# Kernel optimization log

Hardware: AMD Instinct MI355X
Metric: run time of the kernel (lower is better)

Reference implementation:

```python
import jax, jax.numpy as jnp
import numpy as np

B, S, D, H, F = 2, 2048, 1024, 16, 4096
DH = D // H
EPS = 1e-6


def layer_norm(x, g, b):
    mu = jnp.mean(x, axis=-1, keepdims=True)
    var = jnp.mean(jnp.square(x - mu), axis=-1, keepdims=True)
    return (x - mu) * jax.lax.rsqrt(var + EPS) * g + b


def setup_inputs() -> dict:
    key = jax.random.key(0)
    ks = jax.random.split(key, 12)
    s_in = 1.0 / np.sqrt(D)
    s_ff = 1.0 / np.sqrt(F)
    return {
        "x_enc": jax.random.normal(ks[0], (B, S, D), jnp.float32),
        "x_pos": jax.random.normal(ks[1], (B, S, D), jnp.float32),
        "wq": jax.random.normal(ks[2], (D, D), jnp.float32) * s_in,
        "bq": jnp.zeros((D,), jnp.float32),
        "wk": jax.random.normal(ks[3], (D, D), jnp.float32) * s_in,
        "bk": jnp.zeros((D,), jnp.float32),
        "wv": jax.random.normal(ks[4], (D, D), jnp.float32) * s_in,
        "bv": jnp.zeros((D,), jnp.float32),
        "wc": jax.random.normal(ks[5], (D, D), jnp.float32) * s_in,
        "bc": jnp.zeros((D,), jnp.float32),
        "w1": jax.random.normal(ks[6], (D, F), jnp.float32) * s_in,
        "b1": jnp.zeros((F,), jnp.float32),
        "w2": jax.random.normal(ks[7], (F, D), jnp.float32) * s_ff,
        "b2": jnp.zeros((D,), jnp.float32),
        "g1": jnp.ones((D,), jnp.float32),
        "be1": jnp.zeros((D,), jnp.float32),
        "g2": jnp.ones((D,), jnp.float32),
        "be2": jnp.zeros((D,), jnp.float32),
    }


def reference(x_enc, x_pos, wq, bq, wk, bk, wv, bv, wc, bc, w1, b1, w2, b2, g1, be1, g2, be2):
    x = x_enc + x_pos  # [B,S,D]

    def split_heads(t):  # [B,S,D] -> [B,H,S,DH]
        return t.reshape(B, S, H, DH).transpose(0, 2, 1, 3)

    q = split_heads(x @ wq + bq)
    k = split_heads(x @ wk + bk)
    v = split_heads(x @ wv + bv)

    scale = jax.lax.rsqrt(jnp.asarray(DH, jnp.float32))
    logits = jnp.einsum("bhqd,bhkd->bhqk", q, k) * scale  # [B,H,S,S]
    weights = jax.nn.softmax(logits, axis=-1)
    attn = jnp.einsum("bhqk,bhkd->bhqd", weights, v)  # [B,H,S,DH]
    attn = attn.transpose(0, 2, 1, 3).reshape(B, S, D)
    attn = attn @ wc + bc

    # residual: x + LN(attn_out)   (dropout inactive in eval)
    a = x + layer_norm(attn, g1, be1)
    ffn = jnp.maximum(a @ w1 + b1, 0.0) @ w2 + b2
    out = a + layer_norm(ffn, g2, be2)
    return out
```

## Files before the change

kernel.cpp:

```cpp
#include <hip/hip_runtime.h>
#include <math.h>

#define B_ 2
#define S_ 2048
#define D_ 1024
#define H_ 16
#define F_ 4096

typedef __bf16 bf16_t;
typedef __bf16 bf16x8 __attribute__((ext_vector_type(8)));
typedef __bf16 bf16x4 __attribute__((ext_vector_type(4)));
typedef float f32x4 __attribute__((ext_vector_type(4)));
typedef float f32x16 __attribute__((ext_vector_type(16)));
typedef _Float16 f16x4 __attribute__((ext_vector_type(4)));
typedef _Float16 f16x8 __attribute__((ext_vector_type(8)));
typedef __fp16 h16x2 __attribute__((ext_vector_type(2)));

__device__ __forceinline__ bf16_t f2b(float f) { return (bf16_t)f; }

__device__ __forceinline__ void gld_lds16(const void* g, void* l) {
  __builtin_amdgcn_global_load_lds(
      (const __attribute__((address_space(1))) unsigned int*)g,
      (__attribute__((address_space(3))) unsigned int*)l, 16, 0, 0);
}

__device__ __forceinline__ void transpose_tile(const float* __restrict__ in,
                                               bf16_t* __restrict__ out,
                                               int K, int N, int bx, int by) {
  __shared__ float tile[64][65];
  int k0 = by * 64, n0 = bx * 64;
  int tid = threadIdx.x;
  int col4 = tid & 15;
  int row = tid >> 4;
#pragma unroll
  for (int rr = 0; rr < 4; ++rr) {
    int r = rr * 16 + row;
    float4 v = *reinterpret_cast<const float4*>(in + (size_t)(k0 + r) * N + n0 + col4 * 4);
    tile[r][col4 * 4 + 0] = v.x;
    tile[r][col4 * 4 + 1] = v.y;
    tile[r][col4 * 4 + 2] = v.z;
    tile[r][col4 * 4 + 3] = v.w;
  }
  __syncthreads();
#pragma unroll
  for (int rr = 0; rr < 4; ++rr) {
    int n = rr * 16 + row;
    bf16x4 o;
    o[0] = f2b(tile[col4 * 4 + 0][n]);
    o[1] = f2b(tile[col4 * 4 + 1][n]);
    o[2] = f2b(tile[col4 * 4 + 2][n]);
    o[3] = f2b(tile[col4 * 4 + 3][n]);
    *reinterpret_cast<bf16x4*>(out + (size_t)(n0 + n) * K + k0 + col4 * 4) = o;
  }
}

__global__ __launch_bounds__(256) void prep_kernel(
    const float* __restrict__ xe, const float* __restrict__ xp,
    bf16_t* __restrict__ XB,
    const float* __restrict__ wq, const float* __restrict__ wk,
    const float* __restrict__ wv, const float* __restrict__ wc,
    const float* __restrict__ w1, const float* __restrict__ w2,
    const float* __restrict__ bq, const float* __restrict__ bk,
    const float* __restrict__ bv,
    bf16_t* __restrict__ Wqkvt, bf16_t* __restrict__ wctb,
    bf16_t* __restrict__ w1tb, bf16_t* __restrict__ w2tb,
    float* __restrict__ bqkv) {
  int bid = blockIdx.x;
  if (bid < 4096) {
    int i = bid * 256 + threadIdx.x;
    float4 av = reinterpret_cast<const float4*>(xe)[i];
    float4 bv4 = reinterpret_cast<const float4*>(xp)[i];
    bf16x4 o;
    o[0] = f2b(av.x + bv4.x); o[1] = f2b(av.y + bv4.y);
    o[2] = f2b(av.z + bv4.z); o[3] = f2b(av.w + bv4.w);
    reinterpret_cast<bf16x4*>(XB)[i] = o;
    return;
  }
  int pb = bid - 4096;
  if (pb < 1024) {
    int seg = pb >> 8, local = pb & 255;
    const float* src = seg == 0 ? wq : (seg == 1 ? wk : (seg == 2 ? wv : wc));
    bf16_t* dst = seg == 3 ? wctb : Wqkvt + (size_t)seg * D_ * D_;
    transpose_tile(src, dst, D_, D_, local & 15, local >> 4);
  } else if (pb < 2048) {
    int local = pb - 1024;
    transpose_tile(w1, w1tb, D_, F_, local & 63, local >> 6);
  } else if (pb < 3072) {
    int local = pb - 2048;
    transpose_tile(w2, w2tb, F_, D_, local & 15, local >> 4);
  } else {
    int i = (pb - 3072) * 256 + threadIdx.x;
    const float* src = i < 1024 ? bq : (i < 2048 ? bk : bv);
    bqkv[i] = src[i & 1023];
  }
}


__device__ __forceinline__ void stage_half(const bf16_t* __restrict__ G,
                                           int grow0, int K, int kt,
                                           bf16_t* lb, int tid) {
#pragma unroll
  for (int c = 0; c < 2; ++c) {
    int e = c * 512 + tid;
    int rl = e >> 3, kg = e & 7;
    int kgs = kg ^ (rl & 7);
    gld_lds16(G + (size_t)(grow0 + rl) * K + kt + kgs * 8, lb + e * 8);
  }
}

template <int DBUF, int MH, int SSLOT, int DOWAIT>
__device__ __forceinline__ void gemm_phase4(
    bf16_t* As, bf16_t* Bs, const bf16_t* __restrict__ A,
    const bf16_t* __restrict__ Bt, f32x16 (&acc)[4][2], bf16x8 (&bq)[2][4],
    int bm, int bn, int K, int kt, int tid, int m32, int khalf,
    int ra0, int ra1, int rb) {
  stage_half(A, bm + (SSLOT & 1) * 128, K, kt, As + SSLOT * 8192, tid);
  stage_half(Bt, bn + (SSLOT & 1) * 128, K, kt, Bs + SSLOT * 8192, tid);
  const bf16_t* abase = As + (DBUF * 2 + MH) * 8192;
  const bf16_t* b0 = Bs + (DBUF * 2 + 0) * 8192;
  const bf16_t* b1 = Bs + (DBUF * 2 + 1) * 8192;
  bf16x8 af0[4], af1[4];
#pragma unroll
  for (int kc = 0; kc < 4; ++kc) {
    int kg = ((kc * 2 + khalf) ^ (m32 & 7)) * 8;
    af0[kc] = *reinterpret_cast<const bf16x8*>(abase + ra0 * 64 + kg);
    af1[kc] = *reinterpret_cast<const bf16x8*>(abase + ra1 * 64 + kg);
    if (MH == 0) {
      bq[0][kc] = *reinterpret_cast<const bf16x8*>(b0 + rb * 64 + kg);
      bq[1][kc] = *reinterpret_cast<const bf16x8*>(b1 + rb * 64 + kg);
    }
  }
#pragma unroll
  for (int kc = 0; kc < 4; ++kc) {
    acc[MH * 2 + 0][0] = __builtin_amdgcn_mfma_f32_32x32x16_bf16(
        af0[kc], bq[0][kc], acc[MH * 2 + 0][0], 0, 0, 0);
    acc[MH * 2 + 1][0] = __builtin_amdgcn_mfma_f32_32x32x16_bf16(
        af1[kc], bq[0][kc], acc[MH * 2 + 1][0], 0, 0, 0);
    acc[MH * 2 + 0][1] = __builtin_amdgcn_mfma_f32_32x32x16_bf16(
        af0[kc], bq[1][kc], acc[MH * 2 + 0][1], 0, 0, 0);
    acc[MH * 2 + 1][1] = __builtin_amdgcn_mfma_f32_32x32x16_bf16(
        af1[kc], bq[1][kc], acc[MH * 2 + 1][1], 0, 0, 0);
  }
  if (DOWAIT) asm volatile("s_waitcnt vmcnt(4)" ::: "memory");
  asm volatile("s_waitcnt lgkmcnt(0)" ::: "memory");
  __builtin_amdgcn_s_barrier();
}

__global__ __launch_bounds__(512) void gemm_kernel(
    const bf16_t* __restrict__ A, const bf16_t* __restrict__ Bt,
    const float* __restrict__ bias,
    bf16_t* __restrict__ P0, bf16_t* __restrict__ P1,
    bf16_t* __restrict__ P2, bf16_t* __restrict__ P3,
    _Float16* __restrict__ VTout,
    int M, int N, int K, int relu, int kchunk, int rx, int ry) {
  __shared__ bf16_t As[4 * 8192];
  __shared__ bf16_t Bs[4 * 8192];
  int tid = threadIdx.x;
  int lane = tid & 63, wave = tid >> 6;
  int bx = blockIdx.x, by = blockIdx.y;
  if (rx) {
    int id = by * gridDim.x + bx;
    int j = id & 7, local = id >> 3;
    int regs_x = gridDim.x / rx;
    bx = (j % regs_x) * rx + local % rx;
    by = (j / regs_x) * ry + local / rx;
  }
  int bm = by * 256, bn = bx * 256;
  int wm = wave >> 2, wn = wave & 3;
  int m32 = lane & 31, khalf = lane >> 5;
  int ra0 = wm * 64 + m32, ra1 = ra0 + 32, rb = wn * 32 + m32;
  int z = blockIdx.z;
  int kbeg = z * kchunk;
  int nt = kchunk >> 6, ntm1 = nt - 1;
  f32x16 acc[4][2] = {};

  stage_half(A, bm, K, kbeg, As + 0 * 8192, tid);
  stage_half(Bt, bn, K, kbeg, Bs + 0 * 8192, tid);
  stage_half(A, bm + 128, K, kbeg, As + 1 * 8192, tid);
  stage_half(Bt, bn + 128, K, kbeg, Bs + 1 * 8192, tid);
  stage_half(A, bm, K, kbeg + 64, As + 2 * 8192, tid);
  stage_half(Bt, bn, K, kbeg + 64, Bs + 2 * 8192, tid);
  asm volatile("s_waitcnt vmcnt(4)" ::: "memory");
  __builtin_amdgcn_s_barrier();

  int nt2 = nt >> 1;
  for (int j = 0; j < nt2; ++j) {
    int t1 = 2 * j + 1;
    int t2 = 2 * j + 2 > ntm1 ? ntm1 : 2 * j + 2;
    int t3 = 2 * j + 3 > ntm1 ? ntm1 : 2 * j + 3;
    bf16x8 bq[2][4];
    gemm_phase4<0, 0, 3, 0>(As, Bs, A, Bt, acc, bq, bm, bn, K, kbeg + t1 * 64, tid, m32, khalf, ra0, ra1, rb);
    gemm_phase4<0, 1, 0, 1>(As, Bs, A, Bt, acc, bq, bm, bn, K, kbeg + t2 * 64, tid, m32, khalf, ra0, ra1, rb);
    gemm_phase4<1, 0, 1, 0>(As, Bs, A, Bt, acc, bq, bm, bn, K, kbeg + t2 * 64, tid, m32, khalf, ra0, ra1, rb);
    gemm_phase4<1, 1, 2, 1>(As, Bs, A, Bt, acc, bq, bm, bn, K, kbeg + t3 * 64, tid, m32, khalf, ra0, ra1, rb);
  }

  bf16_t* Cb = z == 0 ? P0 : (z == 1 ? P1 : (z == 2 ? P2 : P3));
#pragma unroll
  for (int ni = 0; ni < 2; ++ni) {
    int n = bn + ni * 128 + wn * 32 + m32;
    float bz = (bias && z == 0) ? bias[n] : 0.f;
#pragma unroll
    for (int mi = 0; mi < 4; ++mi) {
      float vv[16];
#pragma unroll
      for (int r = 0; r < 16; ++r) {
        float v = acc[mi][ni][r] + bz;
        if (relu) v = fmaxf(v, 0.f);
        vv[r] = v;
      }
      int sb = bm + (mi >> 1) * 128 + wm * 64 + (mi & 1) * 32;
      if (VTout && n >= 2048) {
        int h = (n - 2048) >> 6, d = (n - 2048) & 63;
        int bb = sb >> 11;
        _Float16* vtr = VTout + ((size_t)((bb * H_ + h) * 64 + d)) * S_ + (sb & 2047);
#pragma unroll
        for (int g = 0; g < 4; ++g) {
          int off = ((2 * g + khalf) & 3) * 8 + (g >> 1) * 4;
          f16x4 hv;
          hv[0] = (_Float16)vv[g * 4 + 0]; hv[1] = (_Float16)vv[g * 4 + 1];
          hv[2] = (_Float16)vv[g * 4 + 2]; hv[3] = (_Float16)vv[g * 4 + 3];
          *reinterpret_cast<f16x4*>(vtr + off) = hv;
        }
      } else {
#pragma unroll
        for (int r = 0; r < 16; ++r) {
          int m = sb + (r & 3) + 8 * (r >> 2) + 4 * khalf;
          Cb[(size_t)m * N + n] = f2b(vv[r]);
        }
      }
    }
  }
}

__device__ __forceinline__ f16x8 softmax8(f32x4 se, f32x4 so, float kS,
                                          float kB, float& lsum, h16x2 one2) {
  float pe0 = __builtin_amdgcn_exp2f(fmaf(se[0], kS, -kB));
  float pe1 = __builtin_amdgcn_exp2f(fmaf(se[1], kS, -kB));
  float pe2 = __builtin_amdgcn_exp2f(fmaf(se[2], kS, -kB));
  float pe3 = __builtin_amdgcn_exp2f(fmaf(se[3], kS, -kB));
  float po0 = __builtin_amdgcn_exp2f(fmaf(so[0], kS, -kB));
  float po1 = __builtin_amdgcn_exp2f(fmaf(so[1], kS, -kB));
  float po2 = __builtin_amdgcn_exp2f(fmaf(so[2], kS, -kB));
  float po3 = __builtin_amdgcn_exp2f(fmaf(so[3], kS, -kB));
  h16x2 e01 = __builtin_amdgcn_cvt_pkrtz(pe0, pe1);
  h16x2 e23 = __builtin_amdgcn_cvt_pkrtz(pe2, pe3);
  h16x2 q01 = __builtin_amdgcn_cvt_pkrtz(po0, po1);
  h16x2 q23 = __builtin_amdgcn_cvt_pkrtz(po2, po3);
  lsum = __builtin_amdgcn_fdot2(e01, one2, lsum, false);
  lsum = __builtin_amdgcn_fdot2(e23, one2, lsum, false);
  lsum = __builtin_amdgcn_fdot2(q01, one2, lsum, false);
  lsum = __builtin_amdgcn_fdot2(q23, one2, lsum, false);
  union { h16x2 h[4]; f16x8 v; } pu;
  pu.h[0] = e01; pu.h[1] = e23; pu.h[2] = q01; pu.h[3] = q23;
  return pu.v;
}

__global__ __launch_bounds__(512) void attn_kernel(const bf16_t* __restrict__ Q,
                                                   const bf16_t* __restrict__ Kg,
                                                   const _Float16* __restrict__ VT,
                                                   bf16_t* __restrict__ O, int ldq) {
  __shared__ bf16_t Ks[2][128 * 64];
  __shared__ _Float16 Vs[2][64 * 128];
  int pid = blockIdx.x + gridDim.x * (blockIdx.y + gridDim.y * blockIdx.z);
  int nid = (pid & 7) * 32 + (pid >> 3);
  int qt = nid & 7, h = (nid >> 3) & 15, b = nid >> 7;
  int tid = threadIdx.x, wave = tid >> 6, lane = tid & 63;
  int qcol = lane & 15, grp = lane >> 4;
  int qbase = qt * 256 + wave * 32;
  const float kS = 0.125f * 1.4426950408889634f;
  const float kB = 12.0f * 1.4426950408889634f;
  const h16x2 one2 = {(__fp16)1.f, (__fp16)1.f};

  bf16x8 qf[2][2];
#pragma unroll
  for (int qi = 0; qi < 2; ++qi)
#pragma unroll
    for (int c = 0; c < 2; ++c)
      qf[qi][c] = *reinterpret_cast<const bf16x8*>(
          Q + (size_t)(b * S_ + qbase + qi * 16 + qcol) * ldq + h * 64 + c * 32 + grp * 8);
  const _Float16* vtb = VT + (size_t)((b * H_ + h) * 64) * S_;

  f32x4 oacc[2][4] = {};
  float lsum[2] = {0.f, 0.f};

#define ATTN_STAGE(BUF, T0)                                                     \
  {                                                                             \
    _Pragma("unroll") for (int cc = 0; cc < 2; ++cc) {                          \
      int e = cc * 512 + tid;                                                   \
      int row = e >> 3, kg = e & 7, kgs = kg ^ (row & 7);                       \
      gld_lds16(Kg + (size_t)(b * S_ + (T0) + row) * ldq + h * 64 + kgs * 8,    \
                &Ks[BUF][0] + e * 8);                                           \
    }                                                                           \
    _Pragma("unroll") for (int cc = 0; cc < 2; ++cc) {                          \
      int e = cc * 512 + tid;                                                   \
      int d = e >> 4, kc = e & 15, kcs = kc ^ (d & 7);                          \
      gld_lds16(vtb + (size_t)d * S_ + (T0) + kcs * 8, &Vs[BUF][0] + e * 8);    \
    }                                                                           \
  }

  ATTN_STAGE(0, 0);
  __syncthreads();

  int buf = 0;
  for (int t0 = 0; t0 < S_; t0 += 128) {
    if (t0 + 128 < S_) {
      if (buf == 0) ATTN_STAGE(1, t0 + 128) else ATTN_STAGE(0, t0 + 128);
    }
    const bf16_t* ksb = &Ks[buf][0];
    const _Float16* vsb = &Vs[buf][0];
#pragma unroll
    for (int kb2 = 0; kb2 < 4; ++kb2) {
      f32x4 se[2] = {}, so[2] = {};
      int krowe = kb2 * 32 + qcol;
      int krowo = krowe + 16;
#pragma unroll
      for (int c = 0; c < 2; ++c) {
        int gce = (c * 4 + grp) ^ (krowe & 7);
        bf16x8 kfe = *reinterpret_cast<const bf16x8*>(ksb + krowe * 64 + gce * 8);
        int gco = (c * 4 + grp) ^ (krowo & 7);
        bf16x8 kfo = *reinterpret_cast<const bf16x8*>(ksb + krowo * 64 + gco * 8);
#pragma unroll
        for (int qi = 0; qi < 2; ++qi) {
          se[qi] = __builtin_amdgcn_mfma_f32_16x16x32_bf16(kfe, qf[qi][c], se[qi], 0, 0, 0);
          so[qi] = __builtin_amdgcn_mfma_f32_16x16x32_bf16(kfo, qf[qi][c], so[qi], 0, 0, 0);
        }
      }
      f16x8 pf0 = softmax8(se[0], so[0], kS, kB, lsum[0], one2);
      f16x8 pf1 = softmax8(se[1], so[1], kS, kB, lsum[1], one2);
      __builtin_amdgcn_s_setprio(1);
#pragma unroll
      for (int db = 0; db < 4; ++db) {
        int d = db * 16 + qcol;
        int kc = (kb2 * 4 + grp) ^ (d & 7);
        f16x8 vf = *reinterpret_cast<const f16x8*>(vsb + d * 128 + kc * 8);
        oacc[0][db] = __builtin_amdgcn_mfma_f32_16x16x32_f16(vf, pf0, oacc[0][db], 0, 0, 0);
        oacc[1][db] = __builtin_amdgcn_mfma_f32_16x16x32_f16(vf, pf1, oacc[1][db], 0, 0, 0);
      }
      __builtin_amdgcn_s_setprio(0);
    }
    __syncthreads();
    buf ^= 1;
  }
#undef ATTN_STAGE

#pragma unroll
  for (int qi = 0; qi < 2; ++qi) {
    float l = lsum[qi];
    l += __shfl_xor(l, 16, 64);
    l += __shfl_xor(l, 32, 64);
    float inv = 1.f / l;
    size_t rowbase = (size_t)(b * S_ + qbase + qi * 16 + qcol) * D_ + h * 64;
#pragma unroll
    for (int db = 0; db < 4; ++db) {
      bf16x4 ov;
      ov[0] = f2b(oacc[qi][db][0] * inv);
      ov[1] = f2b(oacc[qi][db][1] * inv);
      ov[2] = f2b(oacc[qi][db][2] * inv);
      ov[3] = f2b(oacc[qi][db][3] * inv);
      *reinterpret_cast<bf16x4*>(O + rowbase + db * 16 + grp * 4) = ov;
    }
  }
}

__global__ __launch_bounds__(256) void ln_res_kernel(const bf16_t* Y0,
                                                     const bf16_t* Y1,
                                                     const bf16_t* Y2,
                                                     const bf16_t* Y3,
                                                     int nY,
                                                     const bf16_t* Xres,
                                                     const float* __restrict__ g,
                                                     const float* __restrict__ be,
                                                     float* OutF,
                                                     bf16_t* OutB) {
  int row = blockIdx.x;
  int tid = threadIdx.x, wave = tid >> 6, lane = tid & 63;
  size_t base = (size_t)row * D_;
  bf16x4 y0 = reinterpret_cast<const bf16x4*>(Y0 + base)[tid];
  bf16x4 y1 = reinterpret_cast<const bf16x4*>(Y1 + base)[tid];
  float4 v;
  v.x = (float)y0[0] + (float)y1[0];
  v.y = (float)y0[1] + (float)y1[1];
  v.z = (float)y0[2] + (float)y1[2];
  v.w = (float)y0[3] + (float)y1[3];
  if (nY == 4) {
    bf16x4 y2 = reinterpret_cast<const bf16x4*>(Y2 + base)[tid];
    bf16x4 y3 = reinterpret_cast<const bf16x4*>(Y3 + base)[tid];
    v.x += (float)y2[0] + (float)y3[0];
    v.y += (float)y2[1] + (float)y3[1];
    v.z += (float)y2[2] + (float)y3[2];
    v.w += (float)y2[3] + (float)y3[3];
  }
  float s = v.x + v.y + v.z + v.w;
  float s2 = v.x * v.x + v.y * v.y + v.z * v.z + v.w * v.w;
#pragma unroll
  for (int off = 32; off > 0; off >>= 1) {
    s += __shfl_xor(s, off, 64);
    s2 += __shfl_xor(s2, off, 64);
  }
  __shared__ float red[2][4];
  if (lane == 0) { red[0][wave] = s; red[1][wave] = s2; }
  __syncthreads();
  s = red[0][0] + red[0][1] + red[0][2] + red[0][3];
  s2 = red[1][0] + red[1][1] + red[1][2] + red[1][3];
  float mu = s * (1.f / D_);
  float var = s2 * (1.f / D_) - mu * mu;
  float rstd = rsqrtf(var + 1e-6f);
  bf16x4 xr4 = reinterpret_cast<const bf16x4*>(Xres + base)[tid];
  float4 gv = reinterpret_cast<const float4*>(g)[tid];
  float4 bv = reinterpret_cast<const float4*>(be)[tid];
  float4 o;
  o.x = (float)xr4[0] + (v.x - mu) * rstd * gv.x + bv.x;
  o.y = (float)xr4[1] + (v.y - mu) * rstd * gv.y + bv.y;
  o.z = (float)xr4[2] + (v.z - mu) * rstd * gv.z + bv.z;
  o.w = (float)xr4[3] + (v.w - mu) * rstd * gv.w + bv.w;
  if (OutF) reinterpret_cast<float4*>(OutF + base)[tid] = o;
  if (OutB) {
    bf16x4 ob; ob[0] = f2b(o.x); ob[1] = f2b(o.y); ob[2] = f2b(o.z); ob[3] = f2b(o.w);
    reinterpret_cast<bf16x4*>(OutB + base)[tid] = ob;
  }
}

extern "C" void kernel_launch(void* const* d_in, const int* in_sizes, int n_in,
                              void* d_out, int out_size, void* d_ws, size_t ws_size,
                              hipStream_t stream) {
  const float* x_enc = (const float*)d_in[0];
  const float* x_pos = (const float*)d_in[1];
  const float* wq = (const float*)d_in[2];
  const float* bq = (const float*)d_in[3];
  const float* wk = (const float*)d_in[4];
  const float* bk = (const float*)d_in[5];
  const float* wv = (const float*)d_in[6];
  const float* bv = (const float*)d_in[7];
  const float* wc = (const float*)d_in[8];
  const float* bc = (const float*)d_in[9];
  const float* w1 = (const float*)d_in[10];
  const float* b1 = (const float*)d_in[11];
  const float* w2 = (const float*)d_in[12];
  const float* b2 = (const float*)d_in[13];
  const float* g1 = (const float*)d_in[14];
  const float* be1 = (const float*)d_in[15];
  const float* g2 = (const float*)d_in[16];
  const float* be2 = (const float*)d_in[17];

  const size_t MB = 1024ull * 1024ull;
  char* w = (char*)d_ws;
  bf16_t* F0 = (bf16_t*)(w + 0);
  bf16_t* F1p = (bf16_t*)(w + 8 * MB);
  bf16_t* Wqkvt = (bf16_t*)(w + 32 * MB);
  bf16_t* wctb = (bf16_t*)(w + 38 * MB);
  bf16_t* w1tb = (bf16_t*)(w + 40 * MB);
  bf16_t* w2tb = (bf16_t*)(w + 48 * MB);
  bf16_t* XB = (bf16_t*)(w + 56 * MB);
  bf16_t* QKVB = (bf16_t*)(w + 64 * MB);
  bf16_t* Pp0 = (bf16_t*)(w + 64 * MB);
  bf16_t* Pp1 = (bf16_t*)(w + 72 * MB);
  bf16_t* Pp2 = (bf16_t*)(w + 80 * MB);
  bf16_t* F2 = (bf16_t*)(w + 64 * MB);
  bf16_t* F3 = (bf16_t*)(w + 72 * MB);
  bf16_t* ATTNB = (bf16_t*)(w + 88 * MB);
  float* bqkv = (float*)(w + 96 * MB);
  _Float16* VTg = (_Float16*)(w + 104 * MB);
  bf16_t* Pp3 = (bf16_t*)(w + 104 * MB);
  bf16_t* F1B = (bf16_t*)(w + 112 * MB);

  const int rows = B_ * S_;

  prep_kernel<<<7180, 256, 0, stream>>>(x_enc, x_pos, XB,
                                        wq, wk, wv, wc, w1, w2, bq, bk, bv,
                                        Wqkvt, wctb, w1tb, w2tb, bqkv);

  gemm_kernel<<<dim3(3 * D_ / 256, rows / 256, 1), 512, 0, stream>>>(
      XB, Wqkvt, bqkv, QKVB, nullptr, nullptr, nullptr, VTg,
      rows, 3 * D_, D_, 0, D_, 3, 8);

  attn_kernel<<<dim3(S_ / 256, H_, B_), 512, 0, stream>>>(
      QKVB, QKVB + D_, VTg, ATTNB, 3 * D_);

  gemm_kernel<<<dim3(D_ / 256, rows / 256, 4), 512, 0, stream>>>(
      ATTNB, wctb, bc, Pp0, Pp1, Pp2, Pp3, nullptr,
      rows, D_, D_, 0, D_ / 4, 2, 4);

  ln_res_kernel<<<rows, 256, 0, stream>>>(Pp0, Pp1, Pp2, Pp3, 4, XB, g1, be1,
                                          nullptr, XB);

  gemm_kernel<<<dim3(F_ / 256, rows / 256, 1), 512, 0, stream>>>(
      XB, w1tb, b1, F1B, nullptr, nullptr, nullptr, nullptr,
      rows, F_, D_, 1, D_, 4, 8);

  gemm_kernel<<<dim3(D_ / 256, rows / 256, 4), 512, 0, stream>>>(
      F1B, w2tb, b2, F0, F1p, F2, F3, nullptr,
      rows, D_, F_, 0, F_ / 4, 2, 4);

  ln_res_kernel<<<rows, 256, 0, stream>>>(F0, F1p, F2, F3, 4, XB, g2, be2,
                                          (float*)d_out, nullptr);
}
```

Baseline: 337.7 us.

## Replace pipelined 256x256 GEMM with simple single-buffered 128x256 tile kernel

```diff
diff --git a/kernel.cpp b/kernel.cpp
--- a/kernel.cpp
+++ b/kernel.cpp
@@ -108,53 +108,15 @@
   }
 }
 
-template <int DBUF, int MH, int SSLOT, int DOWAIT>
-__device__ __forceinline__ void gemm_phase4(
-    bf16_t* As, bf16_t* Bs, const bf16_t* __restrict__ A,
-    const bf16_t* __restrict__ Bt, f32x16 (&acc)[4][2], bf16x8 (&bq)[2][4],
-    int bm, int bn, int K, int kt, int tid, int m32, int khalf,
-    int ra0, int ra1, int rb) {
-  stage_half(A, bm + (SSLOT & 1) * 128, K, kt, As + SSLOT * 8192, tid);
-  stage_half(Bt, bn + (SSLOT & 1) * 128, K, kt, Bs + SSLOT * 8192, tid);
-  const bf16_t* abase = As + (DBUF * 2 + MH) * 8192;
-  const bf16_t* b0 = Bs + (DBUF * 2 + 0) * 8192;
-  const bf16_t* b1 = Bs + (DBUF * 2 + 1) * 8192;
-  bf16x8 af0[4], af1[4];
-#pragma unroll
-  for (int kc = 0; kc < 4; ++kc) {
-    int kg = ((kc * 2 + khalf) ^ (m32 & 7)) * 8;
-    af0[kc] = *reinterpret_cast<const bf16x8*>(abase + ra0 * 64 + kg);
-    af1[kc] = *reinterpret_cast<const bf16x8*>(abase + ra1 * 64 + kg);
-    if (MH == 0) {
-      bq[0][kc] = *reinterpret_cast<const bf16x8*>(b0 + rb * 64 + kg);
-      bq[1][kc] = *reinterpret_cast<const bf16x8*>(b1 + rb * 64 + kg);
-    }
-  }
-#pragma unroll
-  for (int kc = 0; kc < 4; ++kc) {
-    acc[MH * 2 + 0][0] = __builtin_amdgcn_mfma_f32_32x32x16_bf16(
-        af0[kc], bq[0][kc], acc[MH * 2 + 0][0], 0, 0, 0);
-    acc[MH * 2 + 1][0] = __builtin_amdgcn_mfma_f32_32x32x16_bf16(
-        af1[kc], bq[0][kc], acc[MH * 2 + 1][0], 0, 0, 0);
-    acc[MH * 2 + 0][1] = __builtin_amdgcn_mfma_f32_32x32x16_bf16(
-        af0[kc], bq[1][kc], acc[MH * 2 + 0][1], 0, 0, 0);
-    acc[MH * 2 + 1][1] = __builtin_amdgcn_mfma_f32_32x32x16_bf16(
-        af1[kc], bq[1][kc], acc[MH * 2 + 1][1], 0, 0, 0);
-  }
-  if (DOWAIT) asm volatile("s_waitcnt vmcnt(4)" ::: "memory");
-  asm volatile("s_waitcnt lgkmcnt(0)" ::: "memory");
-  __builtin_amdgcn_s_barrier();
-}
-
-__global__ __launch_bounds__(512) void gemm_kernel(
+__global__ __launch_bounds__(512, 4) void gemm_kernel(
     const bf16_t* __restrict__ A, const bf16_t* __restrict__ Bt,
     const float* __restrict__ bias,
     bf16_t* __restrict__ P0, bf16_t* __restrict__ P1,
     bf16_t* __restrict__ P2, bf16_t* __restrict__ P3,
     _Float16* __restrict__ VTout,
     int M, int N, int K, int relu, int kchunk, int rx, int ry) {
-  __shared__ bf16_t As[4 * 8192];
-  __shared__ bf16_t Bs[4 * 8192];
+  __shared__ bf16_t As[128 * 64];
+  __shared__ bf16_t Bs[256 * 64];
   int tid = threadIdx.x;
   int lane = tid & 63, wave = tid >> 6;
   int bx = blockIdx.x, by = blockIdx.y;
@@ -165,43 +127,56 @@
     bx = (j % regs_x) * rx + local % rx;
     by = (j / regs_x) * ry + local / rx;
   }
-  int bm = by * 256, bn = bx * 256;
+  int bm = by * 128, bn = bx * 256;
   int wm = wave >> 2, wn = wave & 3;
   int m32 = lane & 31, khalf = lane >> 5;
-  int ra0 = wm * 64 + m32, ra1 = ra0 + 32, rb = wn * 32 + m32;
+  int ra0 = wm * 64 + m32, ra1 = ra0 + 32;
+  int rb0 = wn * 64 + m32, rb1 = rb0 + 32;
   int z = blockIdx.z;
-  int kbeg = z * kchunk;
-  int nt = kchunk >> 6, ntm1 = nt - 1;
-  f32x16 acc[4][2] = {};
-
-  stage_half(A, bm, K, kbeg, As + 0 * 8192, tid);
-  stage_half(Bt, bn, K, kbeg, Bs + 0 * 8192, tid);
-  stage_half(A, bm + 128, K, kbeg, As + 1 * 8192, tid);
-  stage_half(Bt, bn + 128, K, kbeg, Bs + 1 * 8192, tid);
-  stage_half(A, bm, K, kbeg + 64, As + 2 * 8192, tid);
-  stage_half(Bt, bn, K, kbeg + 64, Bs + 2 * 8192, tid);
-  asm volatile("s_waitcnt vmcnt(4)" ::: "memory");
-  __builtin_amdgcn_s_barrier();
-
-  int nt2 = nt >> 1;
-  for (int j = 0; j < nt2; ++j) {
-    int t1 = 2 * j + 1;
-    int t2 = 2 * j + 2 > ntm1 ? ntm1 : 2 * j + 2;
-    int t3 = 2 * j + 3 > ntm1 ? ntm1 : 2 * j + 3;
-    bf16x8 bq[2][4];
-    gemm_phase4<0, 0, 3, 0>(As, Bs, A, Bt, acc, bq, bm, bn, K, kbeg + t1 * 64, tid, m32, khalf, ra0, ra1, rb);
-    gemm_phase4<0, 1, 0, 1>(As, Bs, A, Bt, acc, bq, bm, bn, K, kbeg + t2 * 64, tid, m32, khalf, ra0, ra1, rb);
-    gemm_phase4<1, 0, 1, 0>(As, Bs, A, Bt, acc, bq, bm, bn, K, kbeg + t2 * 64, tid, m32, khalf, ra0, ra1, rb);
-    gemm_phase4<1, 1, 2, 1>(As, Bs, A, Bt, acc, bq, bm, bn, K, kbeg + t3 * 64, tid, m32, khalf, ra0, ra1, rb);
+  int kbeg = z * kchunk, kend = kbeg + kchunk;
+  f32x16 acc[2][2] = {};
+
+  for (int kt = kbeg; kt < kend; kt += 64) {
+    stage_half(A, bm, K, kt, As, tid);
+    stage_half(Bt, bn, K, kt, Bs, tid);
+    stage_half(Bt, bn + 128, K, kt, Bs + 128 * 64, tid);
+    asm volatile("s_waitcnt vmcnt(0)" ::: "memory");
+    __builtin_amdgcn_s_barrier();
+#pragma unroll
+    for (int kc = 0; kc < 4; ++kc) {
+      bf16x8 af0, af1, bf0, bf1;
+      {
+        int kg = ((kc * 2 + khalf) ^ (ra0 & 7)) * 8;
+        af0 = *reinterpret_cast<const bf16x8*>(As + ra0 * 64 + kg);
+      }
+      {
+        int kg = ((kc * 2 + khalf) ^ (ra1 & 7)) * 8;
+        af1 = *reinterpret_cast<const bf16x8*>(As + ra1 * 64 + kg);
+      }
+      {
+        int kg = ((kc * 2 + khalf) ^ (rb0 & 7)) * 8;
+        bf0 = *reinterpret_cast<const bf16x8*>(Bs + rb0 * 64 + kg);
+      }
+      {
+        int kg = ((kc * 2 + khalf) ^ (rb1 & 7)) * 8;
+        bf1 = *reinterpret_cast<const bf16x8*>(Bs + rb1 * 64 + kg);
+      }
+      acc[0][0] = __builtin_amdgcn_mfma_f32_32x32x16_bf16(af0, bf0, acc[0][0], 0, 0, 0);
+      acc[1][0] = __builtin_amdgcn_mfma_f32_32x32x16_bf16(af1, bf0, acc[1][0], 0, 0, 0);
+      acc[0][1] = __builtin_amdgcn_mfma_f32_32x32x16_bf16(af0, bf1, acc[0][1], 0, 0, 0);
+      acc[1][1] = __builtin_amdgcn_mfma_f32_32x32x16_bf16(af1, bf1, acc[1][1], 0, 0, 0);
+    }
+    asm volatile("s_waitcnt lgkmcnt(0)" ::: "memory");
+    __builtin_amdgcn_s_barrier();
   }
 
   bf16_t* Cb = z == 0 ? P0 : (z == 1 ? P1 : (z == 2 ? P2 : P3));
 #pragma unroll
   for (int ni = 0; ni < 2; ++ni) {
-    int n = bn + ni * 128 + wn * 32 + m32;
+    int n = bn + wn * 64 + ni * 32 + m32;
     float bz = (bias && z == 0) ? bias[n] : 0.f;
 #pragma unroll
-    for (int mi = 0; mi < 4; ++mi) {
+    for (int mi = 0; mi < 2; ++mi) {
       float vv[16];
 #pragma unroll
       for (int r = 0; r < 16; ++r) {
@@ -209,7 +184,7 @@
         if (relu) v = fmaxf(v, 0.f);
         vv[r] = v;
       }
-      int sb = bm + (mi >> 1) * 128 + wm * 64 + (mi & 1) * 32;
+      int sb = bm + wm * 64 + mi * 32;
       if (VTout && n >= 2048) {
         int h = (n - 2048) >> 6, d = (n - 2048) & 63;
         int bb = sb >> 11;
@@ -470,27 +445,27 @@
                                         wq, wk, wv, wc, w1, w2, bq, bk, bv,
                                         Wqkvt, wctb, w1tb, w2tb, bqkv);
 
-  gemm_kernel<<<dim3(3 * D_ / 256, rows / 256, 1), 512, 0, stream>>>(
+  gemm_kernel<<<dim3(3 * D_ / 256, rows / 128, 1), 512, 0, stream>>>(
       XB, Wqkvt, bqkv, QKVB, nullptr, nullptr, nullptr, VTg,
-      rows, 3 * D_, D_, 0, D_, 3, 8);
+      rows, 3 * D_, D_, 0, D_, 3, 16);
 
   attn_kernel<<<dim3(S_ / 256, H_, B_), 512, 0, stream>>>(
       QKVB, QKVB + D_, VTg, ATTNB, 3 * D_);
 
-  gemm_kernel<<<dim3(D_ / 256, rows / 256, 4), 512, 0, stream>>>(
+  gemm_kernel<<<dim3(D_ / 256, rows / 128, 4), 512, 0, stream>>>(
       ATTNB, wctb, bc, Pp0, Pp1, Pp2, Pp3, nullptr,
-      rows, D_, D_, 0, D_ / 4, 2, 4);
+      rows, D_, D_, 0, D_ / 4, 1, 16);
 
   ln_res_kernel<<<rows, 256, 0, stream>>>(Pp0, Pp1, Pp2, Pp3, 4, XB, g1, be1,
                                           nullptr, XB);
 
-  gemm_kernel<<<dim3(F_ / 256, rows / 256, 1), 512, 0, stream>>>(
+  gemm_kernel<<<dim3(F_ / 256, rows / 128, 1), 512, 0, stream>>>(
       XB, w1tb, b1, F1B, nullptr, nullptr, nullptr, nullptr,
-      rows, F_, D_, 1, D_, 4, 8);
-
-  gemm_kernel<<<dim3(D_ / 256, rows / 256, 4), 512, 0, stream>>>(
+      rows, F_, D_, 1, D_, 2, 32);
+
+  gemm_kernel<<<dim3(D_ / 256, rows / 128, 4), 512, 0, stream>>>(
       F1B, w2tb, b2, F0, F1p, F2, F3, nullptr,
-      rows, D_, F_, 0, F_ / 4, 2, 4);
+      rows, D_, F_, 0, F_ / 4, 1, 16);
 
   ln_res_kernel<<<rows, 256, 0, stream>>>(F0, F1p, F2, F3, 4, XB, g2, be2,
                                           (float*)d_out, nullptr);
```

Result: slower. 346.4 us (+2.6%).
